# Optimization experiments

Measured on AMD Instinct MI355X. Metric: run time of the kernel, lower is better.

Reference implementation:

```python
import jax, jax.numpy as jnp
import numpy as np

H, W = 64, 64

def _fft_mask(h, w):
    # matches torch: W -> W//2+1 for rfft; linspace(-1,1,H) x linspace(0,1,W//2+1)
    wr = w // 2 + 1
    ys = np.linspace(-1.0, 1.0, h)
    xs = np.linspace(0.0, 1.0, wr)
    Y, X = np.meshgrid(ys, xs, indexing='ij')
    return (np.abs(X) < 0.1) | (np.abs(Y) < 0.1) | (X ** 2 + Y ** 2 <= 0.4 ** 2)

_MASK = _fft_mask(H, W)
_IY, _IX = np.nonzero(_MASK)            # static gather indices, K = mask.sum()
_K = int(_MASK.sum())


def setup_inputs() -> dict:
    key = jax.random.key(0)
    k1, k2, k3 = jax.random.split(key, 3)
    S, P, C = 16, 256, 3
    enc_dim = 1024
    mask_dim = 6 * _K                    # real+imag, C=3 channels -> 2*3*K
    x = jax.random.normal(k1, (S, P, C, H, W), dtype=jnp.float32)
    bc_mask = jnp.zeros((H, W), dtype=bool)
    proj_w = jax.random.normal(k2, (enc_dim, mask_dim), dtype=jnp.float32) / np.sqrt(mask_dim)
    proj_b = jax.random.normal(k3, (enc_dim,), dtype=jnp.float32) * 0.01
    return {"x": x, "bc_mask": bc_mask, "proj_w": proj_w, "proj_b": proj_b}


def reference(x, bc_mask, proj_w, proj_b):
    S, P, C = x.shape[0], x.shape[1], x.shape[2]
    fft_x = jnp.fft.rfft2(x)                       # (S,P,C,H,W//2+1) complex
    fft_x = jnp.fft.fftshift(fft_x, axes=-2)       # shift along H
    # boolean-mask gather (row-major over (H, W//2+1) per (s,p,c)), then flatten C*K
    filt = fft_x[..., _IY, _IX]                    # (S,P,C,K)
    filt = filt.reshape(S, P, C * _K)
    feats = jnp.concatenate([jnp.real(filt), jnp.imag(filt)], axis=-1)  # (S,P,6K)
    return feats @ proj_w.T + proj_b               # (S,P,enc_dim)
```

## Files before the change

kernel.cpp:

```cpp
#include <hip/hip_runtime.h>
#include <hip/hip_bf16.h>
#include <math.h>

typedef float f32x4 __attribute__((ext_vector_type(4)));
typedef __bf16 bf16x8 __attribute__((ext_vector_type(8)));

#define PI2 6.283185307179586

static __device__ __forceinline__ unsigned short f2b(float f) {
  __hip_bfloat16 h = __float2bfloat16(f);
  return reinterpret_cast<unsigned short&>(h);
}

__global__ __launch_bounds__(256) void setup_tables_kernel(
    unsigned short* __restrict__ post16, __hip_bfloat16* __restrict__ Tt,
    __hip_bfloat16* __restrict__ Ub) {
  const int tid = threadIdx.x;
  __shared__ int cnt[64];
  __shared__ int pref[64];

  if (tid < 64) {
    int i = tid;
    double ys = -1.0 + (double)i * (2.0 / 63.0);
    int cRow = 0;
    for (int j = 0; j < 33; ++j) {
      double xs = (double)j / 32.0;
      bool m = (fabs(xs) < 0.1) || (fabs(ys) < 0.1) || (xs * xs + ys * ys <= 0.16);
      cRow += m ? 1 : 0;
    }
    cnt[i] = cRow;
  }
  __syncthreads();
  if (tid == 0) {
    int s = 0;
    for (int i = 0; i < 64; ++i) { pref[i] = s; s += cnt[i]; }
  }
  __syncthreads();
  if (tid < 64) {
    int i = tid;
    int k = pref[i];
    double ys = -1.0 + (double)i * (2.0 / 63.0);
    for (int j = 0; j < 36; ++j) {
      unsigned short v = 0xFFFFu;
      if (j < 33) {
        double xs = (double)j / 32.0;
        bool m = (fabs(xs) < 0.1) || (fabs(ys) < 0.1) || (xs * xs + ys * ys <= 0.16);
        if (m) v = (unsigned short)(k++);
      }
      post16[i * 36 + j] = v;
    }
  }

  for (int idx = tid; idx < 80 * 64; idx += 256) {
    int n = idx >> 6, w = idx & 63;
    float v = 0.0f;
    if (n < 33) {
      int r = (n * w) & 63;
      v = cosf((float)(PI2 / 64.0) * (float)r);
    } else if (n >= 40 && n < 73) {
      int r = ((n - 40) * w) & 63;
      v = -sinf((float)(PI2 / 64.0) * (float)r);
    }
    Tt[idx] = __float2bfloat16(v);
  }

  for (int idx = tid; idx < 128 * 128; idx += 256) {
    int up = idx >> 7, kk = idx & 127;
    int u = up & 63;
    int vfreq = (u + 32) & 63;
    int h = kk & 63;
    int r = (vfreq * h) & 63;
    float cv, sv;
    __sincosf((float)(PI2 / 64.0) * (float)r, &sv, &cv);
    float val;
    if (up < 64) val = (kk < 64) ? cv : sv;
    else         val = (kk < 64) ? -sv : cv;
    Ub[idx] = __float2bfloat16(val);
  }
}

__global__ __launch_bounds__(256) void wconv_kernel(
    const float* __restrict__ W, __hip_bfloat16* __restrict__ wB,
    int N, int Kd, int Kp) {
  int total = N * Kp;
  for (int idx = blockIdx.x * 256 + threadIdx.x; idx < total; idx += gridDim.x * 256) {
    int e = idx / Kp;
    int f = idx - e * Kp;
    float v = (f < Kd) ? W[(size_t)e * Kd + f] : 0.0f;
    wB[idx] = __float2bfloat16(v);
  }
}

#define WAVES 2
#define WBUF 16384
#define POSTB 4608

__global__ __launch_bounds__(128) void fft_mfma_kernel(
    const float* __restrict__ x,
    const __hip_bfloat16* __restrict__ Tt,
    const __hip_bfloat16* __restrict__ Ub,
    const unsigned short* __restrict__ post16,
    __hip_bfloat16* __restrict__ feats,
    int K, int Kp) {
  __shared__ __align__(16) char lds[WAVES * WBUF + POSTB];
  const int tid = threadIdx.x;
  const int lane = tid & 63;
  const int w = tid >> 6;
  const int l4 = lane & 15;
  const int q = lane >> 4;
  const int img = blockIdx.x * WAVES + w;
  const int sp = img / 3;
  const int c = img - sp * 3;
  char* buf = lds + w * WBUF;
  unsigned short* postl = reinterpret_cast<unsigned short*>(lds + WAVES * WBUF);

  {
    const float* xi = x + (size_t)img * 4096;
    #pragma unroll
    for (int r = 0; r < 16; ++r) {
      const float* g = xi + r * 256 + lane * 4;
      __builtin_amdgcn_global_load_lds(
          (const __attribute__((address_space(1))) void*)g,
          (__attribute__((address_space(3))) void*)(buf + r * 1024), 16, 0, 0);
    }
  }
  {
    const unsigned int* src = reinterpret_cast<const unsigned int*>(post16);
    unsigned int* dst = reinterpret_cast<unsigned int*>(postl);
    for (int i = tid; i < (64 * 36) / 2; i += 128) dst[i] = src[i];
  }
  asm volatile("s_waitcnt vmcnt(0)" ::: "memory");
  __syncthreads();

  #pragma unroll
  for (int r = 0; r < 16; ++r) {
    float4 v = *reinterpret_cast<const float4*>(buf + r * 1024 + lane * 16);
    int h = r * 4 + (lane >> 4);
    int woff = h * 128 + (((l4 >> 1) ^ (h & 7)) * 16 + (l4 & 1) * 8);
    ushort4 b;
    b.x = f2b(v.x); b.y = f2b(v.y); b.z = f2b(v.z); b.w = f2b(v.w);
    *reinterpret_cast<ushort4*>(buf + woff) = b;
  }

  f32x4 acc1[4][5] = {};
  #pragma unroll
  for (int ks = 0; ks < 2; ++ks) {
    bf16x8 a1[4], b1[5];
    #pragma unroll
    for (int m = 0; m < 4; ++m) {
      int h = m * 16 + l4;
      int kg = ks * 4 + q;
      a1[m] = *reinterpret_cast<const bf16x8*>(buf + h * 128 + ((kg ^ (h & 7)) * 16));
    }
    #pragma unroll
    for (int n = 0; n < 5; ++n) {
      int row = n * 16 + l4;
      b1[n] = *reinterpret_cast<const bf16x8*>(
          (const char*)Tt + row * 128 + ks * 64 + q * 16);
    }
    #pragma unroll
    for (int m = 0; m < 4; ++m)
      #pragma unroll
      for (int n = 0; n < 5; ++n)
        acc1[m][n] = __builtin_amdgcn_mfma_f32_16x16x32_bf16(a1[m], b1[n], acc1[m][n], 0, 0, 0);
  }

  #pragma unroll
  for (int n = 0; n < 5; ++n) {
    int col = n * 16 + l4;
    bool isRe = (col < 33);
    bool isIm = (col >= 40 && col < 73);
    if (!(isRe || isIm)) continue;
    int j = isRe ? col : (col - 40);
    #pragma unroll
    for (int m = 0; m < 4; ++m) {
      #pragma unroll
      for (int r = 0; r < 4; ++r) {
        int h = m * 16 + q * 4 + r;
        int kk = isRe ? h : (h + 64);
        int off = j * 256 + (((kk >> 3) ^ (j & 15)) * 16 + (kk & 7) * 2);
        *reinterpret_cast<unsigned short*>(buf + off) = f2b(acc1[m][n][r]);
      }
    }
  }

  f32x4 acc2[3][8] = {};
  #pragma unroll
  for (int ks = 0; ks < 4; ++ks) {
    bf16x8 a2[3], b2[8];
    #pragma unroll
    for (int m = 0; m < 3; ++m) {
      int j = m * 16 + l4;
      if (j > 33) j = 33;
      int kg = ks * 4 + q;
      a2[m] = *reinterpret_cast<const bf16x8*>(buf + j * 256 + ((kg ^ (j & 15)) * 16));
    }
    #pragma unroll
    for (int n = 0; n < 8; ++n) {
      int row = n * 16 + l4;
      b2[n] = *reinterpret_cast<const bf16x8*>(
          (const char*)Ub + row * 256 + ks * 64 + q * 16);
    }
    #pragma unroll
    for (int m = 0; m < 3; ++m)
      #pragma unroll
      for (int n = 0; n < 8; ++n)
        acc2[m][n] = __builtin_amdgcn_mfma_f32_16x16x32_bf16(a2[m], b2[n], acc2[m][n], 0, 0, 0);
  }

  #pragma unroll
  for (int n = 0; n < 8; ++n) {
    int up = n * 16 + l4;
    int u = up & 63;
    int base = (up >> 6) ? K : 0;
    #pragma unroll
    for (int m = 0; m < 3; ++m) {
      int j0 = m * 16 + q * 4;
      if (j0 >= 33) continue;
      ushort4 kv = *reinterpret_cast<const ushort4*>(postl + u * 36 + j0);
      #pragma unroll
      for (int r = 0; r < 4; ++r) {
        int j = j0 + r;
        short k = (short)((&kv.x)[r]);
        if (j < 33 && k >= 0)
          *reinterpret_cast<unsigned short*>(buf + ((int)k + base) * 2) = f2b(acc2[m][n][r]);
      }
    }
  }

  {
    size_t obase = (size_t)sp * Kp;
    const unsigned int* fb = reinterpret_cast<const unsigned int*>(buf);
    unsigned int* gRe = reinterpret_cast<unsigned int*>(feats + obase + (size_t)c * K);
    unsigned int* gIm = reinterpret_cast<unsigned int*>(feats + obase + (size_t)3 * K + (size_t)c * K);
    const int KD2 = K / 2;
    for (int i = lane; i < KD2; i += 64) {
      gRe[i] = fb[i];
      gIm[i] = fb[KD2 + i];
    }
    if (c == 2) {
      unsigned int* gp = reinterpret_cast<unsigned int*>(feats + obase + (size_t)6 * K);
      int padDw = (Kp - 6 * K) / 2;
      for (int i = lane; i < padDw; i += 64) gp[i] = 0u;
    }
  }
}

#define BM 128
#define BN 128
#define BKK 64

__global__ __launch_bounds__(256) void gemm_bias_kernel(
    const __hip_bfloat16* __restrict__ A, const __hip_bfloat16* __restrict__ B,
    const float* __restrict__ bias, float* __restrict__ C,
    int M, int N, int Kp) {
  __shared__ __align__(16) unsigned short As[BM * BKK];
  __shared__ __align__(16) unsigned short Bs[BN * BKK];

  const int tid = threadIdx.x;
  const int lane = tid & 63;
  const int wid = tid >> 6;
  const int wm = wid & 1;
  const int wn = wid >> 1;
  const int nbm = M / BM;
  const int bm = blockIdx.x % nbm;
  const int bn = blockIdx.x / nbm;
  const int row0A = bm * BM;
  const int row0B = bn * BN;

  f32x4 acc[4][4] = {};

  for (int k0 = 0; k0 < Kp; k0 += BKK) {
    #pragma unroll
    for (int i = 0; i < 4; ++i) {
      int qc = i * 256 + tid;
      int r = qc >> 3;
      int cb = (qc & 7) * 16;
      const char* gA = (const char*)A + ((size_t)(row0A + r) * Kp + k0) * 2 + cb;
      const char* gB = (const char*)B + ((size_t)(row0B + r) * Kp + k0) * 2 + cb;
      char* lA = (char*)As + (size_t)(i * 256 + wid * 64) * 16;
      char* lB = (char*)Bs + (size_t)(i * 256 + wid * 64) * 16;
      __builtin_amdgcn_global_load_lds((const __attribute__((address_space(1))) void*)gA,
                                       (__attribute__((address_space(3))) void*)lA, 16, 0, 0);
      __builtin_amdgcn_global_load_lds((const __attribute__((address_space(1))) void*)gB,
                                       (__attribute__((address_space(3))) void*)lB, 16, 0, 0);
    }
    __syncthreads();

    #pragma unroll
    for (int kk = 0; kk < 2; ++kk) {
      bf16x8 afr[4], bfr[4];
      const int ke = kk * 32 + (lane >> 4) * 8;
      #pragma unroll
      for (int m = 0; m < 4; ++m) {
        int rowA = wm * 64 + m * 16 + (lane & 15);
        afr[m] = *reinterpret_cast<const bf16x8*>(&As[rowA * BKK + ke]);
      }
      #pragma unroll
      for (int n = 0; n < 4; ++n) {
        int rowB = wn * 64 + n * 16 + (lane & 15);
        bfr[n] = *reinterpret_cast<const bf16x8*>(&Bs[rowB * BKK + ke]);
      }
      #pragma unroll
      for (int m = 0; m < 4; ++m)
        #pragma unroll
        for (int n = 0; n < 4; ++n)
          acc[m][n] = __builtin_amdgcn_mfma_f32_16x16x32_bf16(afr[m], bfr[n], acc[m][n], 0, 0, 0);
    }
    __syncthreads();
  }

  #pragma unroll
  for (int n = 0; n < 4; ++n) {
    int gcol = row0B + wn * 64 + n * 16 + (lane & 15);
    float bv = bias[gcol];
    #pragma unroll
    for (int m = 0; m < 4; ++m) {
      int grow0 = row0A + wm * 64 + m * 16 + (lane >> 4) * 4;
      #pragma unroll
      for (int r = 0; r < 4; ++r) {
        C[(size_t)(grow0 + r) * N + gcol] = acc[m][n][r] + bv;
      }
    }
  }
}

extern "C" void kernel_launch(void* const* d_in, const int* in_sizes, int n_in,
                              void* d_out, int out_size, void* d_ws, size_t ws_size,
                              hipStream_t stream) {
  const float* x = (const float*)d_in[0];
  const float* W = (const float*)d_in[2];
  const float* bias = (const float*)d_in[3];
  float* out = (float*)d_out;

  const int ENC = in_sizes[3];
  const int Kd = in_sizes[2] / ENC;
  const int K = Kd / 6;
  const int NIMG = in_sizes[0] / 4096;
  const int SP = NIMG / 3;
  const int Kp = (Kd + 63) & ~63;

  char* ws = (char*)d_ws;
  unsigned short* post16 = (unsigned short*)ws;
  __hip_bfloat16* Tt = (__hip_bfloat16*)(ws + 9216);
  __hip_bfloat16* Ub = (__hip_bfloat16*)(ws + 19456);
  __hip_bfloat16* wB = (__hip_bfloat16*)(ws + 52224);
  size_t wBytes = (size_t)ENC * Kp * 2;
  __hip_bfloat16* feats = (__hip_bfloat16*)(ws + 52224 + wBytes);

  setup_tables_kernel<<<1, 256, 0, stream>>>(post16, Tt, Ub);
  wconv_kernel<<<1024, 256, 0, stream>>>(W, wB, ENC, Kd, Kp);
  fft_mfma_kernel<<<NIMG / WAVES, 128, 0, stream>>>(x, Tt, Ub, post16, feats, K, Kp);
  gemm_bias_kernel<<<(SP / BM) * (ENC / BN), 256, 0, stream>>>(feats, wB, bias, out, SP, ENC, Kp);
}
```

Before: 189.0 us.

## Split each image's DFT across two waves with compact LDS layout

Each image is now handled by two cooperating waves instead of one, so blocks go from 128 to 256 threads with two images each. Each wave computes half of the row-DFT tiles and half of the column-DFT output tiles. The input is loaded through registers instead of global_load_lds, and the per-image LDS footprint shrinks, with a separate output staging region. This adds block-level barriers between stages in exchange for more waves in flight, higher occupancy and less serial MFMA work per wave. The goal is better latency hiding in this memory-bound FFT stage.

```diff
diff --git a/kernel.cpp b/kernel.cpp
--- a/kernel.cpp
+++ b/kernel.cpp
@@ -91,66 +91,62 @@
   }
 }
 
-#define WAVES 2
-#define WBUF 16384
+#define IMGB 10880
 #define POSTB 4608
 
-__global__ __launch_bounds__(128) void fft_mfma_kernel(
+__global__ __launch_bounds__(256, 4) void fft_mfma_kernel(
     const float* __restrict__ x,
     const __hip_bfloat16* __restrict__ Tt,
     const __hip_bfloat16* __restrict__ Ub,
     const unsigned short* __restrict__ post16,
     __hip_bfloat16* __restrict__ feats,
     int K, int Kp) {
-  __shared__ __align__(16) char lds[WAVES * WBUF + POSTB];
+  __shared__ __align__(16) char lds[2 * IMGB + POSTB];
   const int tid = threadIdx.x;
   const int lane = tid & 63;
   const int w = tid >> 6;
+  const int wi = w >> 1;
+  const int wp = w & 1;
   const int l4 = lane & 15;
   const int q = lane >> 4;
-  const int img = blockIdx.x * WAVES + w;
+  const int img = blockIdx.x * 2 + wi;
   const int sp = img / 3;
   const int c = img - sp * 3;
-  char* buf = lds + w * WBUF;
-  unsigned short* postl = reinterpret_cast<unsigned short*>(lds + WAVES * WBUF);
-
-  {
-    const float* xi = x + (size_t)img * 4096;
-    #pragma unroll
-    for (int r = 0; r < 16; ++r) {
-      const float* g = xi + r * 256 + lane * 4;
-      __builtin_amdgcn_global_load_lds(
-          (const __attribute__((address_space(1))) void*)g,
-          (__attribute__((address_space(3))) void*)(buf + r * 1024), 16, 0, 0);
-    }
+  char* ibuf = lds + wi * IMGB;
+  unsigned int* fb = (unsigned int*)(ibuf + 8704);
+  unsigned short* fbs = (unsigned short*)fb;
+  unsigned short* postl = (unsigned short*)(lds + 2 * IMGB);
+
+  const float* xi = x + (size_t)img * 4096;
+  float4 st[8];
+  #pragma unroll
+  for (int r = 0; r < 8; ++r) {
+    int row = wp * 32 + r * 4 + q;
+    st[r] = *reinterpret_cast<const float4*>(xi + row * 64 + l4 * 4);
   }
   {
     const unsigned int* src = reinterpret_cast<const unsigned int*>(post16);
     unsigned int* dst = reinterpret_cast<unsigned int*>(postl);
-    for (int i = tid; i < (64 * 36) / 2; i += 128) dst[i] = src[i];
-  }
-  asm volatile("s_waitcnt vmcnt(0)" ::: "memory");
-  __syncthreads();
-
-  #pragma unroll
-  for (int r = 0; r < 16; ++r) {
-    float4 v = *reinterpret_cast<const float4*>(buf + r * 1024 + lane * 16);
-    int h = r * 4 + (lane >> 4);
-    int woff = h * 128 + (((l4 >> 1) ^ (h & 7)) * 16 + (l4 & 1) * 8);
+    for (int i = tid; i < 1152; i += 256) dst[i] = src[i];
+  }
+  #pragma unroll
+  for (int r = 0; r < 8; ++r) {
+    int row = wp * 32 + r * 4 + q;
+    int off = row * 128 + (((l4 >> 1) ^ (row & 7)) * 16 + (l4 & 1) * 8);
     ushort4 b;
-    b.x = f2b(v.x); b.y = f2b(v.y); b.z = f2b(v.z); b.w = f2b(v.w);
-    *reinterpret_cast<ushort4*>(buf + woff) = b;
-  }
-
-  f32x4 acc1[4][5] = {};
+    b.x = f2b(st[r].x); b.y = f2b(st[r].y); b.z = f2b(st[r].z); b.w = f2b(st[r].w);
+    *reinterpret_cast<ushort4*>(ibuf + off) = b;
+  }
+
+  f32x4 acc1[2][5] = {};
   #pragma unroll
   for (int ks = 0; ks < 2; ++ks) {
-    bf16x8 a1[4], b1[5];
-    #pragma unroll
-    for (int m = 0; m < 4; ++m) {
-      int h = m * 16 + l4;
+    bf16x8 a1[2], b1[5];
+    #pragma unroll
+    for (int am = 0; am < 2; ++am) {
+      int h = (wp * 2 + am) * 16 + l4;
       int kg = ks * 4 + q;
-      a1[m] = *reinterpret_cast<const bf16x8*>(buf + h * 128 + ((kg ^ (h & 7)) * 16));
+      a1[am] = *reinterpret_cast<const bf16x8*>(ibuf + h * 128 + ((kg ^ (h & 7)) * 16));
     }
     #pragma unroll
     for (int n = 0; n < 5; ++n) {
@@ -159,11 +155,13 @@
           (const char*)Tt + row * 128 + ks * 64 + q * 16);
     }
     #pragma unroll
-    for (int m = 0; m < 4; ++m)
+    for (int am = 0; am < 2; ++am)
       #pragma unroll
       for (int n = 0; n < 5; ++n)
-        acc1[m][n] = __builtin_amdgcn_mfma_f32_16x16x32_bf16(a1[m], b1[n], acc1[m][n], 0, 0, 0);
-  }
+        acc1[am][n] = __builtin_amdgcn_mfma_f32_16x16x32_bf16(a1[am], b1[n], acc1[am][n], 0, 0, 0);
+  }
+
+  __syncthreads();
 
   #pragma unroll
   for (int n = 0; n < 5; ++n) {
@@ -173,75 +171,77 @@
     if (!(isRe || isIm)) continue;
     int j = isRe ? col : (col - 40);
     #pragma unroll
-    for (int m = 0; m < 4; ++m) {
+    for (int am = 0; am < 2; ++am) {
       #pragma unroll
       for (int r = 0; r < 4; ++r) {
-        int h = m * 16 + q * 4 + r;
+        int h = (wp * 2 + am) * 16 + q * 4 + r;
         int kk = isRe ? h : (h + 64);
         int off = j * 256 + (((kk >> 3) ^ (j & 15)) * 16 + (kk & 7) * 2);
-        *reinterpret_cast<unsigned short*>(buf + off) = f2b(acc1[m][n][r]);
-      }
-    }
-  }
-
-  f32x4 acc2[3][8] = {};
+        *reinterpret_cast<unsigned short*>(ibuf + off) = f2b(acc1[am][n][r]);
+      }
+    }
+  }
+
+  __syncthreads();
+
+  f32x4 acc2[3][4] = {};
   #pragma unroll
   for (int ks = 0; ks < 4; ++ks) {
-    bf16x8 a2[3], b2[8];
+    bf16x8 a2[3], b2[4];
     #pragma unroll
     for (int m = 0; m < 3; ++m) {
       int j = m * 16 + l4;
       if (j > 33) j = 33;
       int kg = ks * 4 + q;
-      a2[m] = *reinterpret_cast<const bf16x8*>(buf + j * 256 + ((kg ^ (j & 15)) * 16));
-    }
-    #pragma unroll
-    for (int n = 0; n < 8; ++n) {
-      int row = n * 16 + l4;
+      a2[m] = *reinterpret_cast<const bf16x8*>(ibuf + j * 256 + ((kg ^ (j & 15)) * 16));
+    }
+    #pragma unroll
+    for (int n = 0; n < 4; ++n) {
+      int rowg = (wp * 4 + n) * 16 + l4;
       b2[n] = *reinterpret_cast<const bf16x8*>(
-          (const char*)Ub + row * 256 + ks * 64 + q * 16);
+          (const char*)Ub + rowg * 256 + ks * 64 + q * 16);
     }
     #pragma unroll
     for (int m = 0; m < 3; ++m)
       #pragma unroll
-      for (int n = 0; n < 8; ++n)
+      for (int n = 0; n < 4; ++n)
         acc2[m][n] = __builtin_amdgcn_mfma_f32_16x16x32_bf16(a2[m], b2[n], acc2[m][n], 0, 0, 0);
   }
 
-  #pragma unroll
-  for (int n = 0; n < 8; ++n) {
-    int up = n * 16 + l4;
-    int u = up & 63;
-    int base = (up >> 6) ? K : 0;
+  const int base = wp ? K : 0;
+  #pragma unroll
+  for (int n = 0; n < 4; ++n) {
+    int u = n * 16 + l4;
     #pragma unroll
     for (int m = 0; m < 3; ++m) {
       int j0 = m * 16 + q * 4;
-      if (j0 >= 33) continue;
+      if (j0 > 32) continue;
       ushort4 kv = *reinterpret_cast<const ushort4*>(postl + u * 36 + j0);
       #pragma unroll
       for (int r = 0; r < 4; ++r) {
         int j = j0 + r;
-        short k = (short)((&kv.x)[r]);
-        if (j < 33 && k >= 0)
-          *reinterpret_cast<unsigned short*>(buf + ((int)k + base) * 2) = f2b(acc2[m][n][r]);
-      }
-    }
-  }
+        unsigned short k = (&kv.x)[r];
+        if (j < 33 && k != 0xFFFFu)
+          fbs[base + k] = f2b(acc2[m][n][r]);
+      }
+    }
+  }
+
+  __syncthreads();
 
   {
     size_t obase = (size_t)sp * Kp;
-    const unsigned int* fb = reinterpret_cast<const unsigned int*>(buf);
     unsigned int* gRe = reinterpret_cast<unsigned int*>(feats + obase + (size_t)c * K);
     unsigned int* gIm = reinterpret_cast<unsigned int*>(feats + obase + (size_t)3 * K + (size_t)c * K);
     const int KD2 = K / 2;
-    for (int i = lane; i < KD2; i += 64) {
+    for (int i = wp * 64 + lane; i < KD2; i += 128) {
       gRe[i] = fb[i];
       gIm[i] = fb[KD2 + i];
     }
-    if (c == 2) {
+    if (wp == 0 && c == 2) {
       unsigned int* gp = reinterpret_cast<unsigned int*>(feats + obase + (size_t)6 * K);
       int padDw = (Kp - 6 * K) / 2;
-      for (int i = lane; i < padDw; i += 64) gp[i] = 0u;
+      if (lane < padDw) gp[lane] = 0u;
     }
   }
 }
@@ -350,6 +350,6 @@
 
   setup_tables_kernel<<<1, 256, 0, stream>>>(post16, Tt, Ub);
   wconv_kernel<<<1024, 256, 0, stream>>>(W, wB, ENC, Kd, Kp);
-  fft_mfma_kernel<<<NIMG / WAVES, 128, 0, stream>>>(x, Tt, Ub, post16, feats, K, Kp);
+  fft_mfma_kernel<<<NIMG / 2, 256, 0, stream>>>(x, Tt, Ub, post16, feats, K, Kp);
   gemm_bias_kernel<<<(SP / BM) * (ENC / BN), 256, 0, stream>>>(feats, wB, bias, out, SP, ENC, Kp);
 }
```

Result: no change. 191.7 us (+1.4%).
